# Performance work log

Measured on AMD Instinct MI355X. Metric: run time of the kernel, lower is better.

Reference implementation:

```python
import jax, jax.numpy as jnp
import numpy as np
import math

B, D, H, W, C = 1, 16, 56, 56, 256
WD, WH, WW = 2, 7, 7
NH, NP = 8, 4
N = WD * WH * WW          # 98 tokens per window
HD = C // NH
NWIN = (D // WD) * (H // WH) * (W // WW)  # 512


def layernorm(x, g, b, eps=1e-5):
    m = x.mean(-1, keepdims=True)
    v = jnp.mean((x - m) ** 2, -1, keepdims=True)
    return (x - m) * jax.lax.rsqrt(v + eps) * g + b


def _reference_points():
    zz = (jnp.arange(WD, dtype=jnp.float32) + 0.5) / WD
    yy = (jnp.arange(WH, dtype=jnp.float32) + 0.5) / WH
    xx = (jnp.arange(WW, dtype=jnp.float32) + 0.5) / WW
    gz, gy, gx = jnp.meshgrid(zz, yy, xx, indexing='ij')
    return jnp.stack([gx.ravel(), gy.ravel(), gz.ravel()], -1)  # (N, 3) in xyz order


def _trilinear(value, loc):
    # value: (Bn, N, NH, HD); loc: (Bn, N, NH, NP, 3) normalized xyz in [0,1]
    # grid_sample semantics: align_corners=False, zero padding
    Bn = value.shape[0]
    v = value.transpose(0, 2, 1, 3)  # (Bn, NH, S, HD), S == N (window volume)
    px = loc[..., 0] * WW - 0.5
    py = loc[..., 1] * WH - 0.5
    pz = loc[..., 2] * WD - 0.5
    x0, y0, z0 = jnp.floor(px), jnp.floor(py), jnp.floor(pz)
    out = jnp.zeros(loc.shape[:-1] + (HD,), value.dtype)
    for dz in (0, 1):
        for dy in (0, 1):
            for dx in (0, 1):
                xi, yi, zi = x0 + dx, y0 + dy, z0 + dz
                wgt = (1 - jnp.abs(px - xi)) * (1 - jnp.abs(py - yi)) * (1 - jnp.abs(pz - zi))
                valid = ((xi >= 0) & (xi < WW) & (yi >= 0) & (yi < WH) & (zi >= 0) & (zi < WD)).astype(value.dtype)
                idx = (jnp.clip(zi, 0, WD - 1) * (WH * WW) + jnp.clip(yi, 0, WH - 1) * WW
                       + jnp.clip(xi, 0, WW - 1)).astype(jnp.int32)  # (Bn, N, NH, NP)
                idxf = idx.transpose(0, 2, 1, 3).reshape(Bn, NH, N * NP)
                g = jnp.take_along_axis(v, idxf[..., None], axis=2)  # (Bn, NH, N*NP, HD)
                g = g.reshape(Bn, NH, N, NP, HD).transpose(0, 2, 1, 3, 4)
                out = out + g * (wgt * valid)[..., None]
    return out  # (Bn, N, NH, NP, HD)


def setup_inputs():
    key = jax.random.key(0)
    ks = jax.random.split(key, 12)

    def lin(k, fin, fout):
        s = 1.0 / np.sqrt(fin)
        kw, kb = jax.random.split(k)
        return (jax.random.uniform(kw, (fin, fout), jnp.float32, -s, s),
                jax.random.uniform(kb, (fout,), jnp.float32, -s, s))

    val_w, val_b = lin(ks[2], C, C)
    off_w, off_b = lin(ks[3], C, NH * NP * 3)
    aw_w, aw_b = lin(ks[4], C, NH * NP)
    out_w, out_b = lin(ks[5], C, C)
    proj_w, proj_b = lin(ks[6], C, C)
    fc1_w, fc1_b = lin(ks[7], C, 4 * C)
    fc2_w, fc2_b = lin(ks[8], 4 * C, C)
    return dict(
        x=jax.random.normal(ks[0], (B, D, H, W, C), jnp.float32),
        mask=jax.random.uniform(ks[1], (NWIN, N, WD, WH, WW), jnp.float32),
        norm1_g=jnp.ones((C,), jnp.float32), norm1_b=jnp.zeros((C,), jnp.float32),
        val_w=val_w, val_b=val_b, off_w=off_w, off_b=off_b,
        aw_w=aw_w, aw_b=aw_b, out_w=out_w, out_b=out_b,
        anorm_g=jnp.ones((C,), jnp.float32), anorm_b=jnp.zeros((C,), jnp.float32),
        proj_w=proj_w, proj_b=proj_b,
        norm2_g=jnp.ones((C,), jnp.float32), norm2_b=jnp.zeros((C,), jnp.float32),
        fc1_w=fc1_w, fc1_b=fc1_b, fc2_w=fc2_w, fc2_b=fc2_b)


def reference(x, mask, norm1_g, norm1_b, val_w, val_b, off_w, off_b, aw_w, aw_b,
              out_w, out_b, anorm_g, anorm_b, proj_w, proj_b,
              norm2_g, norm2_b, fc1_w, fc1_b, fc2_w, fc2_b):
    shortcut = x
    xn = layernorm(x, norm1_g, norm1_b)
    # window partition (dims divisible by window, shift_size = 0 -> no pad/roll)
    xw = xn.reshape(B, D // WD, WD, H // WH, WH, W // WW, WW, C)
    xw = xw.transpose(0, 1, 3, 5, 2, 4, 6, 7).reshape(-1, N, C)  # (B*NWIN, N, C)
    Bn = B * NWIN
    # --- PositionEmbeddingSine over the per-window mask ---
    z_e = jnp.cumsum(mask, 2) * mask / math.pi
    y_e = jnp.cumsum(mask, 3) * mask / math.pi
    x_e = jnp.cumsum(mask, 4) * mask / math.pi
    emb = mask * (jnp.sin(x_e) + jnp.sin(math.pi * y_e) + z_e)
    emb = emb.reshape(NWIN, N, N)  # flatten(2); N == WD*WH*WW
    diag = jnp.diagonal(emb, axis1=1, axis2=2)  # (NWIN, N)
    q = (xw.reshape(B, NWIN, N, C) + diag[None, :, :, None]).reshape(Bn, N, C)
    # --- MS3DDeformAttn over single level = window ---
    ref = _reference_points()  # (N, 3)
    value = (xw @ val_w + val_b).reshape(Bn, N, NH, HD)
    off = (q @ off_w + off_b).reshape(Bn, N, NH, NP, 3)
    aw = jax.nn.softmax((q @ aw_w + aw_b).reshape(Bn, N, NH, NP), axis=-1)
    loc = ref[None, :, None, None, :] + off / jnp.array([WW, WH, WD], jnp.float32)
    sampled = _trilinear(value, loc)                       # (Bn, N, NH, NP, HD)
    attn = (sampled * aw[..., None]).sum(3).reshape(Bn, N, C) @ out_w + out_b
    # WindowAttention3D epilogue: proj(norm(x + attn))
    xw = layernorm(xw + attn, anorm_g, anorm_b) @ proj_w + proj_b
    # window reverse
    xr = xw.reshape(B, D // WD, H // WH, W // WW, WD, WH, WW, C)
    xr = xr.transpose(0, 1, 4, 2, 5, 3, 6, 7).reshape(B, D, H, W, C)
    x = shortcut + xr
    # MLP branch
    h = layernorm(x, norm2_g, norm2_b)
    h = jax.nn.gelu(h @ fc1_w + fc1_b)
    return x + (h @ fc2_w + fc2_b)
```

## Files before the change

### kernel.cpp

```cpp
#include <hip/hip_runtime.h>
#include <hip/hip_bf16.h>
#include <hip/hip_fp16.h>

#define B2F(x) __bfloat162float(x)
#define F2B(x) __float2bfloat16(x)

typedef __bf16 bf16x8 __attribute__((ext_vector_type(8)));
typedef float floatx4 __attribute__((ext_vector_type(4)));

static constexpr int MROWS = 50176;
static constexpr int CDIM  = 256;
static constexpr int MCHUNK = 25088;

enum { MODE_BF16 = 0, MODE_VALOFFAW = 1, MODE_REVERSE = 3, MODE_GELU = 4, MODE_FC2 = 5 };

#if defined(__has_builtin)
#if __has_builtin(__builtin_amdgcn_global_load_lds)
#define HAS_GLL 1
#endif
#endif
#ifndef HAS_GLL
#define HAS_GLL 0
#endif


__device__ __forceinline__ void win_decode(int r, int& tok) {
    int w = r / 98, n = r - w * 98;
    int dB = w >> 6, hB = (w >> 3) & 7, wB = w & 7;
    int z = n / 49, n2 = n - z * 49, yy = n2 / 7, xx = n2 - yy * 7;
    tok = ((dB * 2 + z) * 56 + hB * 7 + yy) * 56 + wB * 7 + xx;
}

__device__ __forceinline__ float bf2f(unsigned short u) {
    return __uint_as_float(((unsigned)u) << 16);
}

__device__ __forceinline__ float wave_sum64(float v) {
#pragma unroll
    for (int off = 32; off > 0; off >>= 1) v += __shfl_xor(v, off, 64);
    return v;
}


__global__ __launch_bounds__(256) void transpose_all(
    const float* __restrict__ val_w, const float* __restrict__ off_w,
    const float* __restrict__ aw_w,  const float* __restrict__ out_w,
    const float* __restrict__ proj_w, const float* __restrict__ fc1_w,
    const float* __restrict__ fc2_w,
    __hip_bfloat16* __restrict__ valT, __hip_bfloat16* __restrict__ offawT,
    __hip_bfloat16* __restrict__ outT, __hip_bfloat16* __restrict__ projT,
    __hip_bfloat16* __restrict__ fc1T, __hip_bfloat16* __restrict__ fc2T) {
    int bid = blockIdx.x;
    const float* src; __hip_bfloat16* dst; int K, N, base;
    if (bid < 256)       { src = val_w;  dst = valT;           K = 256;  N = 256;  base = 0; }
    else if (bid < 352)  { src = off_w;  dst = offawT;         K = 256;  N = 96;   base = 256; }
    else if (bid < 384)  { src = aw_w;   dst = offawT + 96*256; K = 256; N = 32;   base = 352; }
    else if (bid < 640)  { src = out_w;  dst = outT;           K = 256;  N = 256;  base = 384; }
    else if (bid < 896)  { src = proj_w; dst = projT;          K = 256;  N = 256;  base = 640; }
    else if (bid < 1920) { src = fc1_w;  dst = fc1T;           K = 256;  N = 1024; base = 896; }
    else                 { src = fc2_w;  dst = fc2T;           K = 1024; N = 256;  base = 1920; }
    int i = (bid - base) * 256 + threadIdx.x;
    if (i >= K * N) return;
    int nn = i / K, kk = i - nn * K;
    dst[(size_t)nn * K + kk] = F2B(src[(size_t)kk * N + nn]);
}


__global__ __launch_bounds__(256) void diag_colsum_kernel(
    const float* __restrict__ mask, float* __restrict__ diag,
    const __hip_bfloat16* __restrict__ wT, float* __restrict__ csum) {
    if (blockIdx.x == gridDim.x - 1) {
        int n = threadIdx.x;
        if (n < 128) {
            float s = 0.f;
            for (int k = 0; k < 256; ++k) s += B2F(wT[n * 256 + k]);
            csum[n] = s;
        }
        return;
    }
    int r = blockIdx.x * 256 + threadIdx.x;
    int n = r % 98;
    int z = n / 49, n2 = n - z * 49, yy = n2 / 7, xx = n2 - yy * 7;
    const float* mb = mask + (size_t)r * 98;
    float m = mb[z * 49 + yy * 7 + xx];
    float sz = 0.f, sy = 0.f, sx = 0.f;
    for (int k = 0; k <= z; ++k)  sz += mb[k * 49 + yy * 7 + xx];
    for (int k = 0; k <= yy; ++k) sy += mb[z * 49 + k * 7 + xx];
    for (int k = 0; k <= xx; ++k) sx += mb[z * 49 + yy * 7 + k];
    const float PI = 3.14159265358979323846f;
    diag[r] = m * (sinf(sx * m / PI) + sinf(sy * m) + sz * m / PI);
}


__global__ __launch_bounds__(256) void ln1_kernel(
    const float* __restrict__ x,
    const float* __restrict__ g, const float* __restrict__ b,
    __hip_bfloat16* __restrict__ xw) {
    const int lane = threadIdx.x & 63;
    const int r = blockIdx.x * 4 + (threadIdx.x >> 6);
    int tok; win_decode(r, tok);
    const int c0 = lane * 4;
    float4 v = *(const float4*)(x + (size_t)tok * CDIM + c0);
    float mean = wave_sum64(v.x + v.y + v.z + v.w) * (1.f / 256.f);
    float dx = v.x - mean, dy = v.y - mean, dz = v.z - mean, dw = v.w - mean;
    float var = wave_sum64(dx * dx + dy * dy + dz * dz + dw * dw) * (1.f / 256.f);
    float rstd = rsqrtf(var + 1e-5f);
    float4 gg = *(const float4*)(g + c0);
    float4 bb = *(const float4*)(b + c0);
    __hip_bfloat16 ob[4] = { F2B(dx * rstd * gg.x + bb.x), F2B(dy * rstd * gg.y + bb.y),
                             F2B(dz * rstd * gg.z + bb.z), F2B(dw * rstd * gg.w + bb.w) };
    *(ushort4*)(xw + (size_t)r * CDIM + c0) = *(const ushort4*)ob;
}

__global__ __launch_bounds__(256) void ln_a_kernel(
    const __hip_bfloat16* __restrict__ xw, const __hip_bfloat16* __restrict__ attn,
    const float* __restrict__ g, const float* __restrict__ b,
    __hip_bfloat16* a2) {
    const int lane = threadIdx.x & 63;
    const int r = blockIdx.x * 4 + (threadIdx.x >> 6);
    const int c0 = lane * 4;
    const size_t base = (size_t)r * CDIM + c0;
    ushort4 xv = *(const ushort4*)(xw + base);
    ushort4 av = *(const ushort4*)(attn + base);
    float tx = bf2f(xv.x) + bf2f(av.x);
    float ty = bf2f(xv.y) + bf2f(av.y);
    float tz = bf2f(xv.z) + bf2f(av.z);
    float tw = bf2f(xv.w) + bf2f(av.w);
    float mean = wave_sum64(tx + ty + tz + tw) * (1.f / 256.f);
    float dx = tx - mean, dy = ty - mean, dz = tz - mean, dw = tw - mean;
    float var = wave_sum64(dx * dx + dy * dy + dz * dz + dw * dw) * (1.f / 256.f);
    float rstd = rsqrtf(var + 1e-5f);
    float4 gg = *(const float4*)(g + c0);
    float4 bb = *(const float4*)(b + c0);
    __hip_bfloat16 ob[4] = { F2B(dx * rstd * gg.x + bb.x), F2B(dy * rstd * gg.y + bb.y),
                             F2B(dz * rstd * gg.z + bb.z), F2B(dw * rstd * gg.w + bb.w) };
    *(ushort4*)((__hip_bfloat16*)a2 + base) = *(const ushort4*)ob;
}

__global__ __launch_bounds__(256) void ln2_kernel(
    const float* __restrict__ xres,
    const float* __restrict__ g, const float* __restrict__ b,
    __hip_bfloat16* __restrict__ hin) {
    const int lane = threadIdx.x & 63;
    const int r = blockIdx.x * 4 + (threadIdx.x >> 6);
    const int c0 = lane * 4;
    float4 v = *(const float4*)(xres + (size_t)r * CDIM + c0);
    float mean = wave_sum64(v.x + v.y + v.z + v.w) * (1.f / 256.f);
    float dx = v.x - mean, dy = v.y - mean, dz = v.z - mean, dw = v.w - mean;
    float var = wave_sum64(dx * dx + dy * dy + dz * dz + dw * dw) * (1.f / 256.f);
    float rstd = rsqrtf(var + 1e-5f);
    float4 gg = *(const float4*)(g + c0);
    float4 bb = *(const float4*)(b + c0);
    __hip_bfloat16 ob[4] = { F2B(dx * rstd * gg.x + bb.x), F2B(dy * rstd * gg.y + bb.y),
                             F2B(dz * rstd * gg.z + bb.z), F2B(dw * rstd * gg.w + bb.w) };
    *(ushort4*)(hin + (size_t)r * CDIM + c0) = *(const ushort4*)ob;
}


__global__ __launch_bounds__(512) void sample_fused(
    const __half* __restrict__ offaw,
    const __hip_bfloat16* __restrict__ value,
    __hip_bfloat16* __restrict__ ai) {
    __shared__ __align__(16) __hip_bfloat16 vs[98 * 256];
    __shared__ __align__(16) __half ws[98 * 8 * 32];
    __shared__ __align__(16) unsigned char isb[98 * 8 * 32];
    const int tid = threadIdx.x;
    const int w = blockIdx.x;

    {
        const uint4* vsrc = (const uint4*)(value + (size_t)w * 98 * CDIM);
        uint4* vdst = (uint4*)vs;
#pragma unroll 2
        for (int i = tid; i < 98 * CDIM / 8; i += 512) vdst[i] = vsrc[i];
    }

    for (int u = tid; u < 98 * 8; u += 512) {
        int r = u >> 3, h = u & 7;
        int z = r / 49, n2 = r - z * 49, yy = n2 / 7, xx = n2 - yy * 7;
        const __half* orow = offaw + ((size_t)w * 98 + r) * 128;
        float l0 = __half2float(orow[96 + h * 4 + 0]);
        float l1 = __half2float(orow[96 + h * 4 + 1]);
        float l2 = __half2float(orow[96 + h * 4 + 2]);
        float l3 = __half2float(orow[96 + h * 4 + 3]);
        float mx = fmaxf(fmaxf(l0, l1), fmaxf(l2, l3));
        float e[4];
        e[0] = __expf(l0 - mx); e[1] = __expf(l1 - mx); e[2] = __expf(l2 - mx); e[3] = __expf(l3 - mx);
        float inv = 1.f / (e[0] + e[1] + e[2] + e[3]);
        __half wl[32];
        unsigned char il[32];
#pragma unroll
        for (int p = 0; p < 4; ++p) {
            float ox = __half2float(orow[h * 12 + p * 3 + 0]);
            float oy = __half2float(orow[h * 12 + p * 3 + 1]);
            float oz = __half2float(orow[h * 12 + p * 3 + 2]);
            float px = (float)xx + ox, py = (float)yy + oy, pz = (float)z + oz;
            float fx0 = floorf(px), fy0 = floorf(py), fz0 = floorf(pz);
            int ix = (int)fx0, iy = (int)fy0, iz = (int)fz0;
            float fx = px - fx0, fy = py - fy0, fz = pz - fz0;
            float wp = e[p] * inv;
            int j = 0;
#pragma unroll
            for (int dz = 0; dz < 2; ++dz) {
                int zi = iz + dz;
                float wz = dz ? fz : 1.f - fz;
#pragma unroll
                for (int dy = 0; dy < 2; ++dy) {
                    int yi = iy + dy;
                    float wy = dy ? fy : 1.f - fy;
#pragma unroll
                    for (int dx = 0; dx < 2; ++dx) {
                        int xi = ix + dx;
                        float wxw = dx ? fx : 1.f - fx;
                        bool valid = (zi >= 0) & (zi < 2) & (yi >= 0) & (yi < 7) & (xi >= 0) & (xi < 7);
                        float wc = valid ? wp * wz * wy * wxw : 0.f;
                        int zc = min(max(zi, 0), 1), yc = min(max(yi, 0), 6), xc = min(max(xi, 0), 6);
                        wl[p * 8 + j] = __float2half(wc);
                        il[p * 8 + j] = (unsigned char)(zc * 49 + yc * 7 + xc);
                        ++j;
                    }
                }
            }
        }
        uint4* wd = (uint4*)(ws + (size_t)u * 32);
        const uint4* ws4 = (const uint4*)wl;
#pragma unroll
        for (int q = 0; q < 4; ++q) wd[q] = ws4[q];
        uint4* idd = (uint4*)(isb + (size_t)u * 32);
        const uint4* is4 = (const uint4*)il;
#pragma unroll
        for (int q = 0; q < 2; ++q) idd[q] = is4[q];
    }
    __syncthreads();

    const int c4 = tid & 63;
    const int h = c4 >> 3;
    const int c0 = c4 * 4;
    for (int r = tid >> 6; r < 98; r += 8) {
        const __half* wrow = ws + ((size_t)((r << 3) + h)) * 32;
        const unsigned char* irow = isb + ((size_t)((r << 3) + h)) * 32;
        float a0 = 0.f, a1 = 0.f, a2 = 0.f, a3 = 0.f;
#pragma unroll
        for (int p = 0; p < 4; ++p) {
            uint4 wq = *(const uint4*)(wrow + p * 8);
            uint2 iq = *(const uint2*)(irow + p * 8);
            const __half* wh = (const __half*)&wq;
            const unsigned char* ib = (const unsigned char*)&iq;
#pragma unroll
            for (int j = 0; j < 8; ++j) {
                float wj = __half2float(wh[j]);
                ushort4 v = *(const ushort4*)(vs + (size_t)ib[j] * CDIM + c0);
                a0 += wj * bf2f(v.x);
                a1 += wj * bf2f(v.y);
                a2 += wj * bf2f(v.z);
                a3 += wj * bf2f(v.w);
            }
        }
        __hip_bfloat16 ob[4] = { F2B(a0), F2B(a1), F2B(a2), F2B(a3) };
        *(ushort4*)(ai + ((size_t)w * 98 + r) * CDIM + c0) = *(const ushort4*)ob;
    }
}


template <int MODE>
__global__ __launch_bounds__(256) void gemm_bt(
    const __hip_bfloat16* __restrict__ A,
    const __hip_bfloat16* __restrict__ Bt,
    const int N, const int K,
    const float* __restrict__ bias0,
    const float* __restrict__ bias1,
    const float* __restrict__ bias2,
    void* C,
    void* extra,
    const void* extra2,
    const float* __restrict__ csum) {
    __shared__ __align__(16) __hip_bfloat16 As[2][128 * 32];
    __shared__ __align__(16) __hip_bfloat16 Bs[2][128 * 32];
    const int tid  = threadIdx.x;
    const int lane = tid & 63;
    const int wave = tid >> 6;
    const int wm = (wave >> 1) * 64;
    const int wn = (wave & 1) * 64;
    const int row0 = blockIdx.x * 128;
    const int col0 = blockIdx.y * 128;
    const int l15 = lane & 15;
    const int quad = lane >> 4;

    floatx4 acc[4][4] = {};

    const int sr = tid >> 2;
    const int sk = (tid & 3) * 8;

    const __hip_bfloat16* Ab = A + (size_t)row0 * K + sr * (size_t)K + sk;
    const __hip_bfloat16* Bb = Bt + (size_t)col0 * K + sr * (size_t)K + sk;
    const size_t half64 = (size_t)64 * K;

    auto stage = [&](int buf, int k0) {
#if HAS_GLL
        __builtin_amdgcn_global_load_lds(
            (const __attribute__((address_space(1))) void*)(Ab + k0),
            (__attribute__((address_space(3))) void*)(&As[buf][sr * 32 + sk]), 16, 0, 0);
        __builtin_amdgcn_global_load_lds(
            (const __attribute__((address_space(1))) void*)(Ab + half64 + k0),
            (__attribute__((address_space(3))) void*)(&As[buf][(sr + 64) * 32 + sk]), 16, 0, 0);
        __builtin_amdgcn_global_load_lds(
            (const __attribute__((address_space(1))) void*)(Bb + k0),
            (__attribute__((address_space(3))) void*)(&Bs[buf][sr * 32 + sk]), 16, 0, 0);
        __builtin_amdgcn_global_load_lds(
            (const __attribute__((address_space(1))) void*)(Bb + half64 + k0),
            (__attribute__((address_space(3))) void*)(&Bs[buf][(sr + 64) * 32 + sk]), 16, 0, 0);
#else
        *reinterpret_cast<uint4*>(&As[buf][sr * 32 + sk]) = *reinterpret_cast<const uint4*>(Ab + k0);
        *reinterpret_cast<uint4*>(&As[buf][(sr + 64) * 32 + sk]) = *reinterpret_cast<const uint4*>(Ab + half64 + k0);
        *reinterpret_cast<uint4*>(&Bs[buf][sr * 32 + sk]) = *reinterpret_cast<const uint4*>(Bb + k0);
        *reinterpret_cast<uint4*>(&Bs[buf][(sr + 64) * 32 + sk]) = *reinterpret_cast<const uint4*>(Bb + half64 + k0);
#endif
    };

    const int nk = K >> 5;
    stage(0, 0);
    for (int t = 0; t < nk; ++t) {
        __syncthreads();
        if (t + 1 < nk) stage((t + 1) & 1, (t + 1) * 32);
        const __hip_bfloat16* Asb = As[t & 1];
        const __hip_bfloat16* Bsb = Bs[t & 1];
        bf16x8 af[4], bfg[4];
#pragma unroll
        for (int i = 0; i < 4; ++i)
            af[i] = *reinterpret_cast<const bf16x8*>(&Asb[(wm + i * 16 + l15) * 32 + quad * 8]);
#pragma unroll
        for (int j = 0; j < 4; ++j)
            bfg[j] = *reinterpret_cast<const bf16x8*>(&Bsb[(wn + j * 16 + l15) * 32 + quad * 8]);
#pragma unroll
        for (int i = 0; i < 4; ++i)
#pragma unroll
            for (int j = 0; j < 4; ++j)
                acc[i][j] = __builtin_amdgcn_mfma_f32_16x16x32_bf16(af[i], bfg[j], acc[i][j], 0, 0, 0);
    }

#pragma unroll
    for (int i = 0; i < 4; ++i) {
#pragma unroll
        for (int j = 0; j < 4; ++j) {
#pragma unroll
            for (int rr = 0; rr < 4; ++rr) {
                int row = row0 + wm + i * 16 + quad * 4 + rr;
                int col = col0 + wn + j * 16 + l15;
                float v = acc[i][j][rr];
                if constexpr (MODE == MODE_BF16) {
                    v += bias0[col];
                    ((__hip_bfloat16*)C)[(size_t)row * N + col] = F2B(v);
                } else if constexpr (MODE == MODE_VALOFFAW) {
                    if (col < 256) {
                        v += bias0[col];
                        ((__hip_bfloat16*)C)[(size_t)row * 256 + col] = F2B(v);
                    } else {
                        int c2 = col - 256;
                        const float* diag = (const float*)extra2;
                        v += (c2 < 96 ? bias1[c2] : bias2[c2 - 96]);
                        v += diag[row] * csum[c2];
                        ((__half*)extra)[(size_t)row * 128 + c2] = __float2half(v);
                    }
                } else if constexpr (MODE == MODE_REVERSE) {
                    v += bias0[col];
                    int tok; win_decode(row, tok);
                    const float* xin = (const float*)extra2;
                    ((float*)C)[(size_t)tok * CDIM + col] = xin[(size_t)tok * CDIM + col] + v;
                } else if constexpr (MODE == MODE_GELU) {
                    v += bias0[col];
                    float t2 = 1.5957691216057308f * (v + 0.044715f * v * v * v);
                    v = v / (1.f + __expf(-t2));
                    ((__hip_bfloat16*)C)[(size_t)row * N + col] = F2B(v);
                } else {
                    v += bias0[col];
                    const float* xres = (const float*)extra2;
                    v += xres[(size_t)row * CDIM + col];
                    ((float*)C)[(size_t)row * CDIM + col] = v;
                }
            }
        }
    }
}


extern "C" void kernel_launch(void* const* d_in, const int* in_sizes, int n_in,
                              void* d_out, int out_size, void* d_ws, size_t ws_size,
                              hipStream_t stream) {
    const float* x      = (const float*)d_in[0];
    const float* mask   = (const float*)d_in[1];
    const float* n1g    = (const float*)d_in[2];
    const float* n1b    = (const float*)d_in[3];
    const float* val_w  = (const float*)d_in[4];
    const float* val_b  = (const float*)d_in[5];
    const float* off_w  = (const float*)d_in[6];
    const float* off_b  = (const float*)d_in[7];
    const float* aw_w   = (const float*)d_in[8];
    const float* aw_b   = (const float*)d_in[9];
    const float* out_w  = (const float*)d_in[10];
    const float* out_b  = (const float*)d_in[11];
    const float* ang    = (const float*)d_in[12];
    const float* anb    = (const float*)d_in[13];
    const float* proj_w = (const float*)d_in[14];
    const float* proj_b = (const float*)d_in[15];
    const float* n2g    = (const float*)d_in[16];
    const float* n2b    = (const float*)d_in[17];
    const float* fc1_w  = (const float*)d_in[18];
    const float* fc1_b  = (const float*)d_in[19];
    const float* fc2_w  = (const float*)d_in[20];
    const float* fc2_b  = (const float*)d_in[21];

    char* ws = (char*)d_ws;
    size_t o = 0;
    auto alloc = [&](size_t bytes) {
        size_t r = o;
        o += (bytes + 255) & ~(size_t)255;
        return r;
    };
    const size_t M = MROWS;
    const size_t REGION_B = M * 128 * 2 + M * 256 * 2 + M * 256 * 2;

    __hip_bfloat16* valT    = (__hip_bfloat16*)(ws + alloc(256 * 256 * 2));
    __hip_bfloat16* offawT  = (__hip_bfloat16*)(ws + alloc(128 * 256 * 2));
    __hip_bfloat16* outT    = (__hip_bfloat16*)(ws + alloc(256 * 256 * 2));
    __hip_bfloat16* projT   = (__hip_bfloat16*)(ws + alloc(256 * 256 * 2));
    __hip_bfloat16* fc1T    = (__hip_bfloat16*)(ws + alloc(1024 * 256 * 2));
    __hip_bfloat16* fc2T    = (__hip_bfloat16*)(ws + alloc(256 * 1024 * 2));
    float*          csum    = (float*)(ws + alloc(128 * 4));
    float*          diag    = (float*)(ws + alloc(M * 4));
    char*           slab1   = ws + alloc(M * 256 * 2);
    char*           region  = ws + alloc(REGION_B);
    (void)ws_size; (void)in_sizes; (void)n_in; (void)out_size;

    __hip_bfloat16* xw    = (__hip_bfloat16*)slab1;
    __hip_bfloat16* a2    = (__hip_bfloat16*)slab1;
    __hip_bfloat16* hin   = (__hip_bfloat16*)slab1;
    __half*         offaw = (__half*)region;
    __hip_bfloat16* ai    = (__hip_bfloat16*)(region + M * 128 * 2);
    __hip_bfloat16* hbuf  = (__hip_bfloat16*)region;
    __hip_bfloat16* value = (__hip_bfloat16*)d_out;
    __hip_bfloat16* attn  = (__hip_bfloat16*)d_out;
    float*          xres  = (float*)d_out;

    dim3 blk(256);
    hipLaunchKernelGGL(transpose_all, dim3(2944), blk, 0, stream,
                       val_w, off_w, aw_w, out_w, proj_w, fc1_w, fc2_w,
                       valT, offawT, outT, projT, fc1T, fc2T);
    hipLaunchKernelGGL(diag_colsum_kernel, dim3(MROWS / 256 + 1), blk, 0, stream,
                       mask, diag, offawT, csum);

    hipLaunchKernelGGL(ln1_kernel, dim3(MROWS / 4), blk, 0, stream, x, n1g, n1b, xw);
    hipLaunchKernelGGL((gemm_bt<MODE_VALOFFAW>), dim3(MROWS / 128, 3), blk, 0, stream,
                       xw, valT, 384, 256, val_b, off_b, aw_b,
                       (void*)value, (void*)offaw, (const void*)diag, csum);
    hipLaunchKernelGGL(sample_fused, dim3(MROWS / 98), dim3(512), 0, stream,
                       offaw, value, ai);
    hipLaunchKernelGGL((gemm_bt<MODE_BF16>), dim3(MROWS / 128, 2), blk, 0, stream,
                       ai, outT, 256, 256, out_b, (const float*)nullptr, (const float*)nullptr,
                       (void*)attn, (void*)nullptr, (const void*)nullptr, (const float*)nullptr);
    hipLaunchKernelGGL(ln_a_kernel, dim3(MROWS / 4), blk, 0, stream, xw, attn, ang, anb, a2);
    hipLaunchKernelGGL((gemm_bt<MODE_REVERSE>), dim3(MROWS / 128, 2), blk, 0, stream,
                       a2, projT, 256, 256, proj_b, (const float*)nullptr, (const float*)nullptr,
                       (void*)xres, (void*)nullptr, (const void*)x, (const float*)nullptr);
    hipLaunchKernelGGL(ln2_kernel, dim3(MROWS / 4), blk, 0, stream, xres, n2g, n2b, hin);
    for (int c = 0; c < 2; ++c) {
        const __hip_bfloat16* hin_c = hin + (size_t)c * MCHUNK * 256;
        float*                out_c = (float*)d_out + (size_t)c * MCHUNK * 256;
        hipLaunchKernelGGL((gemm_bt<MODE_GELU>), dim3(MCHUNK / 128, 8), blk, 0, stream,
                           hin_c, fc1T, 1024, 256, fc1_b, (const float*)nullptr, (const float*)nullptr,
                           (void*)hbuf, (void*)nullptr, (const void*)nullptr, (const float*)nullptr);
        hipLaunchKernelGGL((gemm_bt<MODE_FC2>), dim3(MCHUNK / 128, 2), blk, 0, stream,
                           hbuf, fc2T, 256, 1024, fc2_b, (const float*)nullptr, (const float*)nullptr,
                           (void*)out_c, (void*)nullptr, (const void*)out_c, (const float*)nullptr);
    }
}
```

Before: 508.3 us.

## Compute sampling weights per-lane and broadcast via shuffles instead of LDS tables

The deformable sampling kernel no longer builds per-(row,head) weight and index tables in shared memory in a separate phase. Each lane now computes four of the 32 trilinear corner weights for its head and packs index and half-precision weight into one word. The lanes of a head group then exchange these through wavefront shuffles during accumulation. This cuts the LDS footprint (allowing a higher occupancy hint of 6) and spreads the coordinate math across all lanes instead of a few threads. The cost is 32 shuffles per row and redundant softmax computation in every lane.

```diff
diff --git a/kernel.cpp b/kernel.cpp
--- a/kernel.cpp
+++ b/kernel.cpp
@@ -157,98 +157,78 @@
 }
 
 
-__global__ __launch_bounds__(512) void sample_fused(
+__global__ __launch_bounds__(512, 6) void sample_fused(
     const __half* __restrict__ offaw,
     const __hip_bfloat16* __restrict__ value,
     __hip_bfloat16* __restrict__ ai) {
     __shared__ __align__(16) __hip_bfloat16 vs[98 * 256];
-    __shared__ __align__(16) __half ws[98 * 8 * 32];
-    __shared__ __align__(16) unsigned char isb[98 * 8 * 32];
     const int tid = threadIdx.x;
     const int w = blockIdx.x;
 
     {
         const uint4* vsrc = (const uint4*)(value + (size_t)w * 98 * CDIM);
         uint4* vdst = (uint4*)vs;
-#pragma unroll 2
         for (int i = tid; i < 98 * CDIM / 8; i += 512) vdst[i] = vsrc[i];
     }
-
-    for (int u = tid; u < 98 * 8; u += 512) {
-        int r = u >> 3, h = u & 7;
+    __syncthreads();
+
+    const int lane  = tid & 63;
+    const int wave  = tid >> 6;
+    const int h     = lane >> 3;
+    const int s     = lane & 7;
+    const int p     = s >> 1;
+    const int jbase = (s & 1) * 4;
+    const int c0    = lane * 4;
+    const int gbase = lane & ~7;
+
+    for (int r = wave; r < 98; r += 8) {
         int z = r / 49, n2 = r - z * 49, yy = n2 / 7, xx = n2 - yy * 7;
         const __half* orow = offaw + ((size_t)w * 98 + r) * 128;
+
         float l0 = __half2float(orow[96 + h * 4 + 0]);
         float l1 = __half2float(orow[96 + h * 4 + 1]);
         float l2 = __half2float(orow[96 + h * 4 + 2]);
         float l3 = __half2float(orow[96 + h * 4 + 3]);
         float mx = fmaxf(fmaxf(l0, l1), fmaxf(l2, l3));
-        float e[4];
-        e[0] = __expf(l0 - mx); e[1] = __expf(l1 - mx); e[2] = __expf(l2 - mx); e[3] = __expf(l3 - mx);
-        float inv = 1.f / (e[0] + e[1] + e[2] + e[3]);
-        __half wl[32];
-        unsigned char il[32];
-#pragma unroll
-        for (int p = 0; p < 4; ++p) {
-            float ox = __half2float(orow[h * 12 + p * 3 + 0]);
-            float oy = __half2float(orow[h * 12 + p * 3 + 1]);
-            float oz = __half2float(orow[h * 12 + p * 3 + 2]);
-            float px = (float)xx + ox, py = (float)yy + oy, pz = (float)z + oz;
-            float fx0 = floorf(px), fy0 = floorf(py), fz0 = floorf(pz);
-            int ix = (int)fx0, iy = (int)fy0, iz = (int)fz0;
-            float fx = px - fx0, fy = py - fy0, fz = pz - fz0;
-            float wp = e[p] * inv;
-            int j = 0;
-#pragma unroll
-            for (int dz = 0; dz < 2; ++dz) {
-                int zi = iz + dz;
-                float wz = dz ? fz : 1.f - fz;
-#pragma unroll
-                for (int dy = 0; dy < 2; ++dy) {
-                    int yi = iy + dy;
-                    float wy = dy ? fy : 1.f - fy;
-#pragma unroll
-                    for (int dx = 0; dx < 2; ++dx) {
-                        int xi = ix + dx;
-                        float wxw = dx ? fx : 1.f - fx;
-                        bool valid = (zi >= 0) & (zi < 2) & (yi >= 0) & (yi < 7) & (xi >= 0) & (xi < 7);
-                        float wc = valid ? wp * wz * wy * wxw : 0.f;
-                        int zc = min(max(zi, 0), 1), yc = min(max(yi, 0), 6), xc = min(max(xi, 0), 6);
-                        wl[p * 8 + j] = __float2half(wc);
-                        il[p * 8 + j] = (unsigned char)(zc * 49 + yc * 7 + xc);
-                        ++j;
-                    }
-                }
-            }
+        float e0 = __expf(l0 - mx), e1 = __expf(l1 - mx), e2 = __expf(l2 - mx), e3 = __expf(l3 - mx);
+        float inv = 1.f / (e0 + e1 + e2 + e3);
+        float ep = (p == 0) ? e0 : (p == 1) ? e1 : (p == 2) ? e2 : e3;
+        float wp = ep * inv;
+
+        float ox = __half2float(orow[h * 12 + p * 3 + 0]);
+        float oy = __half2float(orow[h * 12 + p * 3 + 1]);
+        float oz = __half2float(orow[h * 12 + p * 3 + 2]);
+        float px = (float)xx + ox, py = (float)yy + oy, pz = (float)z + oz;
+        float fx0 = floorf(px), fy0 = floorf(py), fz0 = floorf(pz);
+        int ix = (int)fx0, iy = (int)fy0, iz = (int)fz0;
+        float fx = px - fx0, fy = py - fy0, fz = pz - fz0;
+
+        uint packed[4];
+#pragma unroll
+        for (int jj = 0; jj < 4; ++jj) {
+            int j = jbase + jj;
+            int dzz = j >> 2, dyy = (j >> 1) & 1, dxx = j & 1;
+            int zi = iz + dzz, yi = iy + dyy, xi = ix + dxx;
+            float wz = dzz ? fz : 1.f - fz;
+            float wy = dyy ? fy : 1.f - fy;
+            float wxw = dxx ? fx : 1.f - fx;
+            bool valid = (zi >= 0) & (zi < 2) & (yi >= 0) & (yi < 7) & (xi >= 0) & (xi < 7);
+            float wc = valid ? wp * wz * wy * wxw : 0.f;
+            int zc = min(max(zi, 0), 1), yc = min(max(yi, 0), 6), xc = min(max(xi, 0), 6);
+            int idx = zc * 49 + yc * 7 + xc;
+            packed[jj] = ((uint)idx << 16) | (uint)__half_as_ushort(__float2half(wc));
         }
-        uint4* wd = (uint4*)(ws + (size_t)u * 32);
-        const uint4* ws4 = (const uint4*)wl;
-#pragma unroll
-        for (int q = 0; q < 4; ++q) wd[q] = ws4[q];
-        uint4* idd = (uint4*)(isb + (size_t)u * 32);
-        const uint4* is4 = (const uint4*)il;
-#pragma unroll
-        for (int q = 0; q < 2; ++q) idd[q] = is4[q];
-    }
-    __syncthreads();
-
-    const int c4 = tid & 63;
-    const int h = c4 >> 3;
-    const int c0 = c4 * 4;
-    for (int r = tid >> 6; r < 98; r += 8) {
-        const __half* wrow = ws + ((size_t)((r << 3) + h)) * 32;
-        const unsigned char* irow = isb + ((size_t)((r << 3) + h)) * 32;
+
         float a0 = 0.f, a1 = 0.f, a2 = 0.f, a3 = 0.f;
 #pragma unroll
-        for (int p = 0; p < 4; ++p) {
-            uint4 wq = *(const uint4*)(wrow + p * 8);
-            uint2 iq = *(const uint2*)(irow + p * 8);
-            const __half* wh = (const __half*)&wq;
-            const unsigned char* ib = (const unsigned char*)&iq;
-#pragma unroll
-            for (int j = 0; j < 8; ++j) {
-                float wj = __half2float(wh[j]);
-                ushort4 v = *(const ushort4*)(vs + (size_t)ib[j] * CDIM + c0);
+        for (int jj = 0; jj < 4; ++jj) {
+            uint mine = packed[jj];
+#pragma unroll
+            for (int sl = 0; sl < 8; ++sl) {
+                uint pk = __shfl(mine, gbase + sl, 64);
+                float wj = __half2float(__ushort_as_half((unsigned short)(pk & 0xffffu)));
+                int idx = (int)(pk >> 16);
+                ushort4 v = *(const ushort4*)(vs + (size_t)idx * CDIM + c0);
                 a0 += wj * bf2f(v.x);
                 a1 += wj * bf2f(v.y);
                 a2 += wj * bf2f(v.z);
```

Result: no change. 514.5 us (+1.2%).
